# Kernel optimization log

Hardware: AMD Instinct MI355X
Metric: run time of the kernel (lower is better)

The kernel has to match this reference:

```python
import jax, jax.numpy as jnp
import numpy as np

N_NODES = 32000
N_EDGES = 320000
N_GRAPHS = 1600
HID = 128
RBF = 32
ZDIM = 2 * HID + RBF  # CGConv concat dim = 288


def setup_inputs() -> dict:
    key = jax.random.key(0)
    ks = jax.random.split(key, 20)
    inp = {
        "x": jax.random.randint(ks[0], (N_NODES,), 0, 100),
        "edge_index": jax.random.randint(ks[1], (2, N_EDGES), 0, N_NODES),
        "edge_attr": jax.random.normal(ks[2], (N_EDGES, RBF), dtype=jnp.float32),
        "batch": jnp.sort(jax.random.randint(ks[3], (N_NODES,), 0, N_GRAPHS)),
        "emb": jax.random.normal(ks[4], (100, HID), dtype=jnp.float32) * 0.02,
    }
    s = 1.0 / np.sqrt(ZDIM)
    for i, k0 in zip((1, 2, 3), range(5, 11, 2)):
        inp[f"Wf{i}"] = jax.random.uniform(ks[k0], (ZDIM, HID), jnp.float32, -s, s)
        inp[f"bf{i}"] = jnp.zeros((HID,), jnp.float32)
        inp[f"Ws{i}"] = jax.random.uniform(ks[k0 + 1], (ZDIM, HID), jnp.float32, -s, s)
        inp[f"bs{i}"] = jnp.zeros((HID,), jnp.float32)
    sl = 1.0 / np.sqrt(HID)
    inp["Wlin"] = jax.random.uniform(ks[11], (HID, HID), jnp.float32, -sl, sl)
    inp["blin"] = jnp.zeros((HID,), jnp.float32)
    return inp


def _cgconv(h, src, dst, ea, Wf, bf, Ws, bs):
    # PyG CGConv: z = [x_i, x_j, e_ij]; msg = sigmoid(lin_f(z)) * softplus(lin_s(z)); out = x + sum_j msg
    z = jnp.concatenate([h[dst], h[src], ea], axis=1)  # [E, 288]
    msg = jax.nn.sigmoid(z @ Wf + bf) * jax.nn.softplus(z @ Ws + bs)  # [E, 128]
    return h + jax.ops.segment_sum(msg, dst, num_segments=N_NODES)


def reference(x, edge_index, edge_attr, batch, emb,
              Wf1, bf1, Ws1, bs1, Wf2, bf2, Ws2, bs2, Wf3, bf3, Ws3, bs3,
              Wlin, blin):
    src, dst = edge_index[0], edge_index[1]
    h = emb[x]  # [N, 128] embedding lookup
    h = jax.nn.relu(_cgconv(h, src, dst, edge_attr, Wf1, bf1, Ws1, bs1))
    h = jax.nn.relu(_cgconv(h, src, dst, edge_attr, Wf2, bf2, Ws2, bs2))
    h = jax.nn.relu(_cgconv(h, src, dst, edge_attr, Wf3, bf3, Ws3, bs3))
    # global mean pool over graphs
    sums = jax.ops.segment_sum(h, batch, num_segments=N_GRAPHS)  # [G, 128]
    cnt = jax.ops.segment_sum(jnp.ones((N_NODES,), h.dtype), batch, num_segments=N_GRAPHS)
    pooled = sums / jnp.maximum(cnt, 1.0)[:, None]
    return pooled @ Wlin + blin  # [G, 128]
```

## Files before the change

kernel.cpp:

```cpp
#include <hip/hip_runtime.h>
#include <math.h>

#define NN 32000
#define NE 320000
#define NG 1600
#define LOG2E 1.4426950408889634f
#define LN2   0.6931471805599453f

using frag_ab = __attribute__((ext_vector_type(8))) short;
using frag_cd = __attribute__((ext_vector_type(4))) float;
typedef float v2f __attribute__((ext_vector_type(2)));

static __device__ __forceinline__ unsigned short f2bf(float f) {
  unsigned u = __builtin_bit_cast(unsigned, f);
  unsigned r = u + 0x7fff + ((u >> 16) & 1);
  return (unsigned short)(r >> 16);
}
static __device__ __forceinline__ float bflo(unsigned u) {
  return __builtin_bit_cast(float, u << 16);
}
static __device__ __forceinline__ float bfhi(unsigned u) {
  return __builtin_bit_cast(float, u & 0xffff0000u);
}
static __device__ __forceinline__ float bfs(unsigned short u) {
  return __builtin_bit_cast(float, (unsigned)u << 16);
}
static __device__ __forceinline__ v2f unpk(unsigned u) {
  return (v2f){bflo(u), bfhi(u)};
}

__global__ __launch_bounds__(256) void k_misc(const int* __restrict__ x,
                                              const float* __restrict__ emb,
                                              const float* __restrict__ Wf1, const float* __restrict__ Ws1,
                                              const float* __restrict__ Wf2, const float* __restrict__ Ws2,
                                              const float* __restrict__ Wf3, const float* __restrict__ Ws3,
                                              unsigned short* __restrict__ hb,
                                              unsigned short* __restrict__ accumb,
                                              unsigned short* __restrict__ wedge,
                                              unsigned short* __restrict__ wgemm) {
  int b = blockIdx.x;
  int tid = threadIdx.x;
  if (b < 2000) {
    int idx = b * 256 + tid;
    int n = idx >> 4;
    int c8 = (idx & 15) << 3;
    const float* e = emb + (size_t)x[n] * 128 + c8;
    float4 v0 = *(const float4*)e;
    float4 v1 = *(const float4*)(e + 4);
    ushort4 p0, p1;
    p0.x = f2bf(v0.x); p0.y = f2bf(v0.y); p0.z = f2bf(v0.z); p0.w = f2bf(v0.w);
    p1.x = f2bf(v1.x); p1.y = f2bf(v1.y); p1.z = f2bf(v1.z); p1.w = f2bf(v1.w);
    unsigned short* hbp = hb + (size_t)n * 128 + c8;
    *(ushort4*)hbp = p0;
    *(ushort4*)(hbp + 4) = p1;
    *(uint4*)(accumb + (size_t)n * 128 + c8) = make_uint4(0, 0, 0, 0);
  } else if (b < 2096) {
    int idx = (b - 2000) * 256 + tid;
    int l = idx >> 13;
    int r = idx & 8191;
    int cc = r >> 5;
    int k = r & 31;
    int w = cc >> 6, t = (cc >> 4) & 3, c = cc & 15;
    const float* Wf = (l == 0) ? Wf1 : (l == 1) ? Wf2 : Wf3;
    const float* Ws = (l == 0) ? Ws1 : (l == 1) ? Ws2 : Ws3;
    const float* W = (t < 2) ? Wf : Ws;
    int ch = w * 32 + 2 * c + (t & 1);
    wedge[(size_t)l * 8192 + cc * 32 + k] = f2bf(W[(size_t)(256 + k) * 128 + ch] * LOG2E);
  } else {
    int idx = (b - 2096) * 256 + tid;
    int l = idx >> 16;
    int r = idx & 65535;
    int cc = r >> 7;
    int k = r & 127;
    int p = (cc & ~31) + ((cc & 15) << 1) + ((cc >> 4) & 1);
    int ph = p & 255;
    int j = ph >> 2, sub = ph & 3;
    const float* Wf = (l == 0) ? Wf1 : (l == 1) ? Wf2 : Wf3;
    const float* Ws = (l == 0) ? Ws1 : (l == 1) ? Ws2 : Ws3;
    const float* W = (sub < 2) ? Wf : Ws;
    int ch = 2 * j + (sub & 1);
    int krow = ((p < 256) ? 0 : 128) + k;
    wgemm[(size_t)l * 65536 + cc * 128 + k] = f2bf(W[(size_t)krow * 128 + ch] * LOG2E);
  }
}

__global__ __launch_bounds__(256) void k_histb(const int* __restrict__ ei,
                                               const int* __restrict__ batch,
                                               int* __restrict__ counts,
                                               int* __restrict__ starts) {
  int b = blockIdx.x;
  int tid = threadIdx.x;
  if (b < 1250) {
    int e = b * 256 + tid;
    atomicAdd(counts + ei[NE + e], 1);
  } else {
    int n = (b - 1250) * 256 + tid;
    if (n > NN) return;
    if (n == NN) {
      starts[NG] = NN;
      int last = batch[NN - 1];
      for (int g = last + 1; g < NG; ++g) starts[g] = NN;
    } else if (n == 0) {
      int bb = batch[0];
      for (int g = 0; g <= bb; ++g) starts[g] = 0;
    } else {
      int b0 = batch[n - 1], b1 = batch[n];
      for (int g = b0 + 1; g <= b1; ++g) starts[g] = n;
    }
  }
}

__global__ __launch_bounds__(1024) void k_scan(const int* __restrict__ counts,
                                               int* __restrict__ offs) {
  __shared__ int part[1024];
  __shared__ int carry_s;
  int t = threadIdx.x;
  if (t == 0) carry_s = 0;
  __syncthreads();
  for (int chunk = 0; chunk < 4; ++chunk) {
    int base = chunk * 8192 + t * 8;
    int4 a = make_int4(0, 0, 0, 0), bq = make_int4(0, 0, 0, 0);
    bool full = (base + 8 <= NN);
    if (full) {
      a = *(const int4*)(counts + base);
      bq = *(const int4*)(counts + base + 4);
    }
    int e1 = a.x, e2 = e1 + a.y, e3 = e2 + a.z, e4 = e3 + a.w;
    int e5 = e4 + bq.x, e6 = e5 + bq.y, e7 = e6 + bq.z;
    int run = e7 + bq.w;
    part[t] = run;
    __syncthreads();
    for (int off = 1; off < 1024; off <<= 1) {
      int v = (t >= off) ? part[t - off] : 0;
      __syncthreads();
      part[t] += v;
      __syncthreads();
    }
    int excl = carry_s + ((t == 0) ? 0 : part[t - 1]);
    if (full) {
      int4 o0 = make_int4(excl, excl + e1, excl + e2, excl + e3);
      int4 o1 = make_int4(excl + e4, excl + e5, excl + e6, excl + e7);
      *(int4*)(offs + base) = o0;
      *(int4*)(offs + base + 4) = o1;
    }
    __syncthreads();
    if (t == 0) carry_s += part[1023];
    __syncthreads();
  }
}

__global__ __launch_bounds__(256) void k_scat1(const int* __restrict__ ei,
                                               int* __restrict__ offs,
                                               int* __restrict__ perm) {
  int e = blockIdx.x * 256 + threadIdx.x;
  int d = ei[NE + e];
  int pos = atomicAdd(offs + d, 1);
  perm[pos] = e;
}

__global__ __launch_bounds__(256) void k_s2g(const unsigned short* __restrict__ hb,
                                             const unsigned short* __restrict__ wgemmL,
                                             unsigned short* __restrict__ T,
                                             const int* __restrict__ ei,
                                             const float* __restrict__ ea,
                                             const int* __restrict__ perm,
                                             int* __restrict__ srcp,
                                             int* __restrict__ dstp,
                                             unsigned short* __restrict__ eab) {
  __shared__ short sA[64 * 136];
  __shared__ short sB[128 * 136];
  __shared__ int se[64];
  int b = blockIdx.x;
  int tid = threadIdx.x;
  if (b < 2000) {
    int m0 = (b >> 2) * 64;
    int n0 = (b & 3) * 128;
#pragma unroll
    for (int i = 0; i < 4; ++i) {
      int idx = tid + i * 256;
      int row = idx >> 4, chk = idx & 15;
      uint4 v = *(const uint4*)(hb + (size_t)(m0 + row) * 128 + chk * 8);
      *(uint4*)&sA[row * 136 + chk * 8] = v;
    }
#pragma unroll
    for (int i = 0; i < 8; ++i) {
      int idx = tid + i * 256;
      int col = idx >> 4, chk = idx & 15;
      uint4 v = *(const uint4*)(wgemmL + (size_t)(n0 + col) * 128 + chk * 8);
      *(uint4*)&sB[col * 136 + chk * 8] = v;
    }
    __syncthreads();
    int w = tid >> 6, lane = tid & 63, c = lane & 15, q = lane >> 4;
    frag_cd acc[4][2];
#pragma unroll
    for (int mt = 0; mt < 4; ++mt)
#pragma unroll
      for (int t = 0; t < 2; ++t) acc[mt][t] = (frag_cd){0.f, 0.f, 0.f, 0.f};
#pragma unroll
    for (int ks = 0; ks < 4; ++ks) {
      frag_ab Af[4], Bf[2];
#pragma unroll
      for (int mt = 0; mt < 4; ++mt)
        Af[mt] = *(const frag_ab*)&sA[(mt * 16 + c) * 136 + ks * 32 + q * 8];
#pragma unroll
      for (int t = 0; t < 2; ++t)
        Bf[t] = *(const frag_ab*)&sB[(w * 32 + t * 16 + c) * 136 + ks * 32 + q * 8];
#pragma unroll
      for (int mt = 0; mt < 4; ++mt)
#pragma unroll
        for (int t = 0; t < 2; ++t)
          acc[mt][t] = __builtin_amdgcn_mfma_f32_16x16x32_bf16(Af[mt], Bf[t], acc[mt][t], 0, 0, 0);
    }
    int nbase = n0 + w * 32 + 2 * c;
#pragma unroll
    for (int mt = 0; mt < 4; ++mt) {
#pragma unroll
      for (int r = 0; r < 4; ++r) {
        int node = m0 + mt * 16 + q * 4 + r;
        unsigned pk = (unsigned)f2bf(acc[mt][0][r]) | ((unsigned)f2bf(acc[mt][1][r]) << 16);
        *(unsigned*)(T + (size_t)node * 512 + nbase) = pk;
      }
    }
  } else {
    int base = (b - 2000) * 64;
    if (tid < 64) {
      int e = perm[base + tid];
      se[tid] = e;
      srcp[base + tid] = ei[e];
      dstp[base + tid] = ei[NE + e];
    }
    __syncthreads();
    int x = tid >> 2;
    int ck = tid & 3;
    int e = se[x];
    const float* a = ea + (size_t)e * 32 + ck * 8;
    float4 v0 = *(const float4*)a;
    float4 v1 = *(const float4*)(a + 4);
    int p = (((x >> 2) & 3) << 4) | ((x >> 4) << 2) | (x & 3);
    unsigned short* q = eab + (size_t)(base + p) * 32 + ck * 8;
    ushort4 o0, o1;
    o0.x = f2bf(v0.x); o0.y = f2bf(v0.y); o0.z = f2bf(v0.z); o0.w = f2bf(v0.w);
    o1.x = f2bf(v1.x); o1.y = f2bf(v1.y); o1.z = f2bf(v1.z); o1.w = f2bf(v1.w);
    *(ushort4*)q = o0;
    *(ushort4*)(q + 4) = o1;
  }
}

__global__ __launch_bounds__(256) void k_gemm(const unsigned short* __restrict__ hb,
                                              const unsigned short* __restrict__ wgemmL,
                                              unsigned short* __restrict__ T) {
  __shared__ short sA[64 * 136];
  __shared__ short sB[128 * 136];
  int m0 = blockIdx.x * 64;
  int n0 = blockIdx.y * 128;
  int tid = threadIdx.x;
#pragma unroll
  for (int i = 0; i < 4; ++i) {
    int idx = tid + i * 256;
    int row = idx >> 4, chk = idx & 15;
    uint4 v = *(const uint4*)(hb + (size_t)(m0 + row) * 128 + chk * 8);
    *(uint4*)&sA[row * 136 + chk * 8] = v;
  }
#pragma unroll
  for (int i = 0; i < 8; ++i) {
    int idx = tid + i * 256;
    int col = idx >> 4, chk = idx & 15;
    uint4 v = *(const uint4*)(wgemmL + (size_t)(n0 + col) * 128 + chk * 8);
    *(uint4*)&sB[col * 136 + chk * 8] = v;
  }
  __syncthreads();
  int w = tid >> 6, lane = tid & 63, c = lane & 15, q = lane >> 4;
  frag_cd acc[4][2];
#pragma unroll
  for (int mt = 0; mt < 4; ++mt)
#pragma unroll
    for (int t = 0; t < 2; ++t) acc[mt][t] = (frag_cd){0.f, 0.f, 0.f, 0.f};
#pragma unroll
  for (int ks = 0; ks < 4; ++ks) {
    frag_ab Af[4], Bf[2];
#pragma unroll
    for (int mt = 0; mt < 4; ++mt)
      Af[mt] = *(const frag_ab*)&sA[(mt * 16 + c) * 136 + ks * 32 + q * 8];
#pragma unroll
    for (int t = 0; t < 2; ++t)
      Bf[t] = *(const frag_ab*)&sB[(w * 32 + t * 16 + c) * 136 + ks * 32 + q * 8];
#pragma unroll
    for (int mt = 0; mt < 4; ++mt)
#pragma unroll
      for (int t = 0; t < 2; ++t)
        acc[mt][t] = __builtin_amdgcn_mfma_f32_16x16x32_bf16(Af[mt], Bf[t], acc[mt][t], 0, 0, 0);
  }
  int nbase = n0 + w * 32 + 2 * c;
#pragma unroll
  for (int mt = 0; mt < 4; ++mt) {
#pragma unroll
    for (int r = 0; r < 4; ++r) {
      int node = m0 + mt * 16 + q * 4 + r;
      unsigned pk = (unsigned)f2bf(acc[mt][0][r]) | ((unsigned)f2bf(acc[mt][1][r]) << 16);
      *(unsigned*)(T + (size_t)node * 512 + nbase) = pk;
    }
  }
}

__global__ __launch_bounds__(256) void k_edge(const int* __restrict__ srcp,
                                              const int* __restrict__ dstp,
                                              const unsigned short* __restrict__ eab,
                                              const unsigned short* __restrict__ T,
                                              const unsigned short* __restrict__ wedgeL,
                                              const float* __restrict__ bf,
                                              const float* __restrict__ bs,
                                              unsigned short* __restrict__ accumb) {
  __shared__ short sA[64 * 40];
  __shared__ short sB[256 * 40];
  __shared__ float sbf[128], sbs[128];
  __shared__ int sSrc[64], sDst[64];
  int tid = threadIdx.x;
  int e0 = blockIdx.x * 64;
  {
    int row = tid >> 2, qq = tid & 3;
    uint4 v = *(const uint4*)(eab + (size_t)e0 * 32 + tid * 8);
    *(uint4*)&sA[row * 40 + qq * 8] = v;
  }
#pragma unroll
  for (int i = 0; i < 4; ++i) {
    int idx = tid + i * 256;
    int col = idx >> 2, qq = idx & 3;
    uint4 v = *(const uint4*)(wedgeL + (size_t)col * 32 + qq * 8);
    *(uint4*)&sB[col * 40 + qq * 8] = v;
  }
  if (tid < 128) {
    sbf[tid] = bf[tid] * LOG2E;
    sbs[tid] = bs[tid] * LOG2E;
  } else if (tid < 192) {
    sSrc[tid - 128] = srcp[e0 + tid - 128] * 512 + 256;
  } else {
    sDst[tid - 192] = dstp[e0 + tid - 192] * 512;
  }
  __syncthreads();

  int w = tid >> 6;
  int lane = tid & 63;
  int c = lane & 15;
  int q = lane >> 4;

  frag_ab Af[4], Bf[4];
#pragma unroll
  for (int et = 0; et < 4; ++et)
    Af[et] = *(const frag_ab*)&sA[(et * 16 + c) * 40 + q * 8];
#pragma unroll
  for (int t = 0; t < 4; ++t)
    Bf[t] = *(const frag_ab*)&sB[(w * 64 + t * 16 + c) * 40 + q * 8];

  frag_cd acc[4][4];
#pragma unroll
  for (int et = 0; et < 4; ++et)
#pragma unroll
    for (int t = 0; t < 4; ++t)
      acc[et][t] = (frag_cd){0.f, 0.f, 0.f, 0.f};
#pragma unroll
  for (int et = 0; et < 4; ++et)
#pragma unroll
    for (int t = 0; t < 4; ++t)
      acc[et][t] = __builtin_amdgcn_mfma_f32_16x16x32_bf16(Af[et], Bf[t], acc[et][t], 0, 0, 0);

  int ch = w * 32 + 2 * c;
  int jo = ch * 2;
  v2f bfv = {sbf[ch], sbf[ch + 1]};
  v2f bsv = {sbs[ch], sbs[ch + 1]};

  int prevd = sDst[q * 16];
  v2f av = {0.f, 0.f};
#pragma unroll
  for (int grp = 0; grp < 2; ++grp) {
    uint2 dv[8], sv[8];
#pragma unroll
    for (int i = 0; i < 8; ++i) {
      int e = q * 16 + grp * 8 + i;
      dv[i] = *(const uint2*)(T + sDst[e] + jo);
      sv[i] = *(const uint2*)(T + sSrc[e] + jo);
    }
    v2f m[8];
#pragma unroll
    for (int i = 0; i < 8; ++i) {
      int idx = grp * 8 + i;
      int et = idx >> 2, r = idx & 3;
      v2f xf = (v2f){acc[et][0][r], acc[et][1][r]} + unpk(dv[i].x) + unpk(sv[i].x) + bfv;
      v2f xs = (v2f){acc[et][2][r], acc[et][3][r]} + unpk(dv[i].y) + unpk(sv[i].y) + bsv;
      float g0 = __builtin_amdgcn_rcpf(1.f + __builtin_amdgcn_exp2f(-xf.x));
      float g1 = __builtin_amdgcn_rcpf(1.f + __builtin_amdgcn_exp2f(-xf.y));
      float sp0 = fmaxf(xs.x, 0.f) + __builtin_amdgcn_logf(1.f + __builtin_amdgcn_exp2f(-fabsf(xs.x)));
      float sp1 = fmaxf(xs.y, 0.f) + __builtin_amdgcn_logf(1.f + __builtin_amdgcn_exp2f(-fabsf(xs.y)));
      m[i] = (v2f){g0 * sp0, g1 * sp1};
    }
#pragma unroll
    for (int i = 0; i < 8; ++i) {
      int d = sDst[q * 16 + grp * 8 + i];
      if (d != prevd) {
        v2f o = av * LN2;
        unsigned pk = (unsigned)f2bf(o.x) | ((unsigned)f2bf(o.y) << 16);
        unsigned short* p = accumb + (size_t)(prevd >> 2) + ch;
        asm volatile("global_atomic_pk_add_bf16 %0, %1, off" :: "v"(p), "v"(pk) : "memory");
        av = (v2f){0.f, 0.f};
        prevd = d;
      }
      av += m[i];
    }
  }
  {
    v2f o = av * LN2;
    unsigned pk = (unsigned)f2bf(o.x) | ((unsigned)f2bf(o.y) << 16);
    unsigned short* p = accumb + (size_t)(prevd >> 2) + ch;
    asm volatile("global_atomic_pk_add_bf16 %0, %1, off" :: "v"(p), "v"(pk) : "memory");
  }
}

__global__ __launch_bounds__(256) void k_update(unsigned short* __restrict__ hb,
                                                unsigned short* __restrict__ accumb) {
  int idx = blockIdx.x * 256 + threadIdx.x;
  size_t off = (size_t)idx * 8;
  uint4 a = *(uint4*)(accumb + off);
  uint4 hv = *(uint4*)(hb + off);
  float r0 = fmaxf(bflo(hv.x) + bflo(a.x), 0.f);
  float r1 = fmaxf(bfhi(hv.x) + bfhi(a.x), 0.f);
  float r2 = fmaxf(bflo(hv.y) + bflo(a.y), 0.f);
  float r3 = fmaxf(bfhi(hv.y) + bfhi(a.y), 0.f);
  float r4 = fmaxf(bflo(hv.z) + bflo(a.z), 0.f);
  float r5 = fmaxf(bfhi(hv.z) + bfhi(a.z), 0.f);
  float r6 = fmaxf(bflo(hv.w) + bflo(a.w), 0.f);
  float r7 = fmaxf(bfhi(hv.w) + bfhi(a.w), 0.f);
  uint4 o;
  o.x = (unsigned)f2bf(r0) | ((unsigned)f2bf(r1) << 16);
  o.y = (unsigned)f2bf(r2) | ((unsigned)f2bf(r3) << 16);
  o.z = (unsigned)f2bf(r4) | ((unsigned)f2bf(r5) << 16);
  o.w = (unsigned)f2bf(r6) | ((unsigned)f2bf(r7) << 16);
  *(uint4*)(hb + off) = o;
  *(uint4*)(accumb + off) = make_uint4(0, 0, 0, 0);
}

__global__ __launch_bounds__(128) void k_pool_final(const unsigned short* __restrict__ hb,
                                                    const unsigned short* __restrict__ accumb,
                                                    const int* __restrict__ starts,
                                                    const float* __restrict__ Wlin,
                                                    const float* __restrict__ blin,
                                                    float* __restrict__ out) {
  __shared__ float p[128];
  int g = blockIdx.x, c = threadIdx.x;
  int s0 = starts[g], s1 = starts[g + 1];
  float acc = 0.f;
  for (int n = s0; n < s1; ++n) {
    float hv = bfs(hb[(size_t)n * 128 + c]);
    float av = bfs(accumb[(size_t)n * 128 + c]);
    acc += fmaxf(hv + av, 0.f);
  }
  float inv = 1.f / fmaxf((float)(s1 - s0), 1.f);
  p[c] = acc * inv;
  __syncthreads();
  float o = blin[c];
#pragma unroll 8
  for (int k = 0; k < 128; ++k) o += p[k] * Wlin[k * 128 + c];
  out[(size_t)g * 128 + c] = o;
}

extern "C" void kernel_launch(void* const* d_in, const int* in_sizes, int n_in,
                              void* d_out, int out_size, void* d_ws, size_t ws_size,
                              hipStream_t stream) {
  const int* x = (const int*)d_in[0];
  const int* ei = (const int*)d_in[1];
  const float* ea = (const float*)d_in[2];
  const int* batch = (const int*)d_in[3];
  const float* emb = (const float*)d_in[4];
  const float* Wf[3] = {(const float*)d_in[5], (const float*)d_in[9], (const float*)d_in[13]};
  const float* bf[3] = {(const float*)d_in[6], (const float*)d_in[10], (const float*)d_in[14]};
  const float* Wsm[3] = {(const float*)d_in[7], (const float*)d_in[11], (const float*)d_in[15]};
  const float* bs[3] = {(const float*)d_in[8], (const float*)d_in[12], (const float*)d_in[16]};
  const float* Wlin = (const float*)d_in[17];
  const float* blin = (const float*)d_in[18];
  float* out = (float*)d_out;

  char* ws = (char*)d_ws;
  unsigned short* hb = (unsigned short*)ws;     ws += (size_t)NN * 128 * 2;
  unsigned short* accumb = (unsigned short*)ws; ws += (size_t)NN * 128 * 2;
  unsigned short* T = (unsigned short*)ws;      ws += (size_t)NN * 512 * 2;
  unsigned short* eab = (unsigned short*)ws;    ws += (size_t)NE * 32 * 2;
  unsigned short* wedge = (unsigned short*)ws;  ws += 3 * 8192 * 2;
  unsigned short* wgemm = (unsigned short*)ws;  ws += 3 * 65536 * 2;
  int* counts = (int*)ws;                       ws += (size_t)NN * 4;
  int* offs = (int*)ws;                         ws += (size_t)NN * 4;
  int* srcp = (int*)ws;                         ws += (size_t)NE * 4;
  int* dstp = (int*)ws;                         ws += (size_t)NE * 4;
  int* perm = (int*)ws;                         ws += (size_t)NE * 4;
  int* starts = (int*)ws;                       ws += (size_t)(NG + 1) * 4;

  hipMemsetAsync(counts, 0, (size_t)NN * 4, stream);
  k_misc<<<2864, 256, 0, stream>>>(x, emb, Wf[0], Wsm[0], Wf[1], Wsm[1], Wf[2], Wsm[2],
                                   hb, accumb, wedge, wgemm);
  k_histb<<<1376, 256, 0, stream>>>(ei, batch, counts, starts);
  k_scan<<<1, 1024, 0, stream>>>(counts, offs);
  k_scat1<<<1250, 256, 0, stream>>>(ei, offs, perm);
  k_s2g<<<7000, 256, 0, stream>>>(hb, wgemm, T, ei, ea, perm, srcp, dstp, eab);
  for (int l = 0; l < 3; ++l) {
    if (l > 0)
      k_gemm<<<dim3(500, 4), 256, 0, stream>>>(hb, wgemm + (size_t)l * 65536, T);
    k_edge<<<5000, 256, 0, stream>>>(srcp, dstp, eab, T, wedge + (size_t)l * 8192,
                                     bf[l], bs[l], accumb);
    if (l < 2)
      k_update<<<2000, 256, 0, stream>>>(hb, accumb);
  }
  k_pool_final<<<1600, 128, 0, stream>>>(hb, accumb, starts, Wlin, blin, out);
}
```

Baseline: 352.1 us.

## Fuse node update into GEMM and load edge weights directly as MFMA fragments

The residual-add+ReLU update kernel is folded into the per-layer node GEMM. Each block now applies the update to its 64 rows, writes hb and clears accumb, keeps the result in shared memory, then loops over all four 128-column weight tiles. This removes a kernel launch and a round trip of hb through memory, but it cuts GEMM grid parallelism from 2000 to 500 blocks. Separately, the edge weight matrix is prepacked in MFMA fragment order so k_edge loads B fragments straight from global memory, dropping the 20KB shared buffer and its staging.

```diff
diff --git a/kernel.cpp b/kernel.cpp
--- a/kernel.cpp
+++ b/kernel.cpp
@@ -58,14 +58,17 @@
     int idx = (b - 2000) * 256 + tid;
     int l = idx >> 13;
     int r = idx & 8191;
-    int cc = r >> 5;
-    int k = r & 31;
-    int w = cc >> 6, t = (cc >> 4) & 3, c = cc & 15;
+    int j = r & 7;
+    int lane = (r >> 3) & 63;
+    int wt = r >> 9;
+    int w = wt >> 2, t = wt & 3;
+    int c = lane & 15, q = lane >> 4;
+    int k = q * 8 + j;
     const float* Wf = (l == 0) ? Wf1 : (l == 1) ? Wf2 : Wf3;
     const float* Ws = (l == 0) ? Ws1 : (l == 1) ? Ws2 : Ws3;
     const float* W = (t < 2) ? Wf : Ws;
     int ch = w * 32 + 2 * c + (t & 1);
-    wedge[(size_t)l * 8192 + cc * 32 + k] = f2bf(W[(size_t)(256 + k) * 128 + ch] * LOG2E);
+    wedge[(size_t)l * 8192 + r] = f2bf(W[(size_t)(256 + k) * 128 + ch] * LOG2E);
   } else {
     int idx = (b - 2096) * 256 + tid;
     int l = idx >> 16;
@@ -246,58 +249,80 @@
   }
 }
 
-__global__ __launch_bounds__(256) void k_gemm(const unsigned short* __restrict__ hb,
-                                              const unsigned short* __restrict__ wgemmL,
-                                              unsigned short* __restrict__ T) {
+__global__ __launch_bounds__(256) void k_ugemm(unsigned short* __restrict__ hb,
+                                               unsigned short* __restrict__ accumb,
+                                               const unsigned short* __restrict__ wgemmL,
+                                               unsigned short* __restrict__ T) {
   __shared__ short sA[64 * 136];
   __shared__ short sB[128 * 136];
   int m0 = blockIdx.x * 64;
-  int n0 = blockIdx.y * 128;
   int tid = threadIdx.x;
 #pragma unroll
   for (int i = 0; i < 4; ++i) {
     int idx = tid + i * 256;
     int row = idx >> 4, chk = idx & 15;
-    uint4 v = *(const uint4*)(hb + (size_t)(m0 + row) * 128 + chk * 8);
-    *(uint4*)&sA[row * 136 + chk * 8] = v;
-  }
-#pragma unroll
-  for (int i = 0; i < 8; ++i) {
-    int idx = tid + i * 256;
-    int col = idx >> 4, chk = idx & 15;
-    uint4 v = *(const uint4*)(wgemmL + (size_t)(n0 + col) * 128 + chk * 8);
-    *(uint4*)&sB[col * 136 + chk * 8] = v;
-  }
-  __syncthreads();
+    size_t off = (size_t)(m0 + row) * 128 + chk * 8;
+    uint4 a = *(uint4*)(accumb + off);
+    uint4 hv = *(uint4*)(hb + off);
+    float r0 = fmaxf(bflo(hv.x) + bflo(a.x), 0.f);
+    float r1 = fmaxf(bfhi(hv.x) + bfhi(a.x), 0.f);
+    float r2 = fmaxf(bflo(hv.y) + bflo(a.y), 0.f);
+    float r3 = fmaxf(bfhi(hv.y) + bfhi(a.y), 0.f);
+    float r4 = fmaxf(bflo(hv.z) + bflo(a.z), 0.f);
+    float r5 = fmaxf(bfhi(hv.z) + bfhi(a.z), 0.f);
+    float r6 = fmaxf(bflo(hv.w) + bflo(a.w), 0.f);
+    float r7 = fmaxf(bfhi(hv.w) + bfhi(a.w), 0.f);
+    uint4 o;
+    o.x = (unsigned)f2bf(r0) | ((unsigned)f2bf(r1) << 16);
+    o.y = (unsigned)f2bf(r2) | ((unsigned)f2bf(r3) << 16);
+    o.z = (unsigned)f2bf(r4) | ((unsigned)f2bf(r5) << 16);
+    o.w = (unsigned)f2bf(r6) | ((unsigned)f2bf(r7) << 16);
+    *(uint4*)(hb + off) = o;
+    *(uint4*)(accumb + off) = make_uint4(0, 0, 0, 0);
+    *(uint4*)&sA[row * 136 + chk * 8] = o;
+  }
   int w = tid >> 6, lane = tid & 63, c = lane & 15, q = lane >> 4;
-  frag_cd acc[4][2];
-#pragma unroll
-  for (int mt = 0; mt < 4; ++mt)
-#pragma unroll
-    for (int t = 0; t < 2; ++t) acc[mt][t] = (frag_cd){0.f, 0.f, 0.f, 0.f};
-#pragma unroll
-  for (int ks = 0; ks < 4; ++ks) {
-    frag_ab Af[4], Bf[2];
+#pragma unroll 1
+  for (int nb = 0; nb < 4; ++nb) {
+    int n0 = nb * 128;
+    __syncthreads();
+#pragma unroll
+    for (int i = 0; i < 8; ++i) {
+      int idx = tid + i * 256;
+      int col = idx >> 4, chk = idx & 15;
+      uint4 v = *(const uint4*)(wgemmL + (size_t)(n0 + col) * 128 + chk * 8);
+      *(uint4*)&sB[col * 136 + chk * 8] = v;
+    }
+    __syncthreads();
+    frag_cd acc[4][2];
 #pragma unroll
     for (int mt = 0; mt < 4; ++mt)
-      Af[mt] = *(const frag_ab*)&sA[(mt * 16 + c) * 136 + ks * 32 + q * 8];
-#pragma unroll
-    for (int t = 0; t < 2; ++t)
-      Bf[t] = *(const frag_ab*)&sB[(w * 32 + t * 16 + c) * 136 + ks * 32 + q * 8];
-#pragma unroll
-    for (int mt = 0; mt < 4; ++mt)
+#pragma unroll
+      for (int t = 0; t < 2; ++t) acc[mt][t] = (frag_cd){0.f, 0.f, 0.f, 0.f};
+#pragma unroll
+    for (int ks = 0; ks < 4; ++ks) {
+      frag_ab Af[4], Bf[2];
+#pragma unroll
+      for (int mt = 0; mt < 4; ++mt)
+        Af[mt] = *(const frag_ab*)&sA[(mt * 16 + c) * 136 + ks * 32 + q * 8];
 #pragma unroll
       for (int t = 0; t < 2; ++t)
-        acc[mt][t] = __builtin_amdgcn_mfma_f32_16x16x32_bf16(Af[mt], Bf[t], acc[mt][t], 0, 0, 0);
-  }
-  int nbase = n0 + w * 32 + 2 * c;
-#pragma unroll
-  for (int mt = 0; mt < 4; ++mt) {
-#pragma unroll
-    for (int r = 0; r < 4; ++r) {
-      int node = m0 + mt * 16 + q * 4 + r;
-      unsigned pk = (unsigned)f2bf(acc[mt][0][r]) | ((unsigned)f2bf(acc[mt][1][r]) << 16);
-      *(unsigned*)(T + (size_t)node * 512 + nbase) = pk;
+        Bf[t] = *(const frag_ab*)&sB[(w * 32 + t * 16 + c) * 136 + ks * 32 + q * 8];
+#pragma unroll
+      for (int mt = 0; mt < 4; ++mt)
+#pragma unroll
+        for (int t = 0; t < 2; ++t)
+          acc[mt][t] = __builtin_amdgcn_mfma_f32_16x16x32_bf16(Af[mt], Bf[t], acc[mt][t], 0, 0, 0);
+    }
+    int nbase = n0 + w * 32 + 2 * c;
+#pragma unroll
+    for (int mt = 0; mt < 4; ++mt) {
+#pragma unroll
+      for (int r = 0; r < 4; ++r) {
+        int node = m0 + mt * 16 + q * 4 + r;
+        unsigned pk = (unsigned)f2bf(acc[mt][0][r]) | ((unsigned)f2bf(acc[mt][1][r]) << 16);
+        *(unsigned*)(T + (size_t)node * 512 + nbase) = pk;
+      }
     }
   }
 }
@@ -311,22 +336,25 @@
                                               const float* __restrict__ bs,
                                               unsigned short* __restrict__ accumb) {
   __shared__ short sA[64 * 40];
-  __shared__ short sB[256 * 40];
   __shared__ float sbf[128], sbs[128];
   __shared__ int sSrc[64], sDst[64];
   int tid = threadIdx.x;
   int e0 = blockIdx.x * 64;
+
+  int w = tid >> 6;
+  int lane = tid & 63;
+  int c = lane & 15;
+  int q = lane >> 4;
+
+  frag_ab Bf[4];
+#pragma unroll
+  for (int t = 0; t < 4; ++t)
+    Bf[t] = *(const frag_ab*)(wedgeL + (((w * 4 + t) * 64 + lane) << 3));
+
   {
     int row = tid >> 2, qq = tid & 3;
     uint4 v = *(const uint4*)(eab + (size_t)e0 * 32 + tid * 8);
     *(uint4*)&sA[row * 40 + qq * 8] = v;
-  }
-#pragma unroll
-  for (int i = 0; i < 4; ++i) {
-    int idx = tid + i * 256;
-    int col = idx >> 2, qq = idx & 3;
-    uint4 v = *(const uint4*)(wedgeL + (size_t)col * 32 + qq * 8);
-    *(uint4*)&sB[col * 40 + qq * 8] = v;
   }
   if (tid < 128) {
     sbf[tid] = bf[tid] * LOG2E;
@@ -338,18 +366,10 @@
   }
   __syncthreads();
 
-  int w = tid >> 6;
-  int lane = tid & 63;
-  int c = lane & 15;
-  int q = lane >> 4;
-
-  frag_ab Af[4], Bf[4];
+  frag_ab Af[4];
 #pragma unroll
   for (int et = 0; et < 4; ++et)
     Af[et] = *(const frag_ab*)&sA[(et * 16 + c) * 40 + q * 8];
-#pragma unroll
-  for (int t = 0; t < 4; ++t)
-    Bf[t] = *(const frag_ab*)&sB[(w * 64 + t * 16 + c) * 40 + q * 8];
 
   frag_cd acc[4][4];
 #pragma unroll
@@ -412,29 +432,6 @@
     unsigned short* p = accumb + (size_t)(prevd >> 2) + ch;
     asm volatile("global_atomic_pk_add_bf16 %0, %1, off" :: "v"(p), "v"(pk) : "memory");
   }
-}
-
-__global__ __launch_bounds__(256) void k_update(unsigned short* __restrict__ hb,
-                                                unsigned short* __restrict__ accumb) {
-  int idx = blockIdx.x * 256 + threadIdx.x;
-  size_t off = (size_t)idx * 8;
-  uint4 a = *(uint4*)(accumb + off);
-  uint4 hv = *(uint4*)(hb + off);
-  float r0 = fmaxf(bflo(hv.x) + bflo(a.x), 0.f);
-  float r1 = fmaxf(bfhi(hv.x) + bfhi(a.x), 0.f);
-  float r2 = fmaxf(bflo(hv.y) + bflo(a.y), 0.f);
-  float r3 = fmaxf(bfhi(hv.y) + bfhi(a.y), 0.f);
-  float r4 = fmaxf(bflo(hv.z) + bflo(a.z), 0.f);
-  float r5 = fmaxf(bfhi(hv.z) + bfhi(a.z), 0.f);
-  float r6 = fmaxf(bflo(hv.w) + bflo(a.w), 0.f);
-  float r7 = fmaxf(bfhi(hv.w) + bfhi(a.w), 0.f);
-  uint4 o;
-  o.x = (unsigned)f2bf(r0) | ((unsigned)f2bf(r1) << 16);
-  o.y = (unsigned)f2bf(r2) | ((unsigned)f2bf(r3) << 16);
-  o.z = (unsigned)f2bf(r4) | ((unsigned)f2bf(r5) << 16);
-  o.w = (unsigned)f2bf(r6) | ((unsigned)f2bf(r7) << 16);
-  *(uint4*)(hb + off) = o;
-  *(uint4*)(accumb + off) = make_uint4(0, 0, 0, 0);
 }
 
 __global__ __launch_bounds__(128) void k_pool_final(const unsigned short* __restrict__ hb,
@@ -500,11 +497,9 @@
   k_s2g<<<7000, 256, 0, stream>>>(hb, wgemm, T, ei, ea, perm, srcp, dstp, eab);
   for (int l = 0; l < 3; ++l) {
     if (l > 0)
-      k_gemm<<<dim3(500, 4), 256, 0, stream>>>(hb, wgemm + (size_t)l * 65536, T);
+      k_ugemm<<<500, 256, 0, stream>>>(hb, accumb, wgemm + (size_t)l * 65536, T);
     k_edge<<<5000, 256, 0, stream>>>(srcp, dstp, eab, T, wedge + (size_t)l * 8192,
                                      bf[l], bs[l], accumb);
-    if (l < 2)
-      k_update<<<2000, 256, 0, stream>>>(hb, accumb);
   }
   k_pool_final<<<1600, 128, 0, stream>>>(hb, accumb, starts, Wlin, blin, out);
 }
```

Measured after the change: 365.5 us. 1.04x slower.
